# Kernel tuning notes

Measured on AMD Instinct MI355X. Metric: run time of the kernel, lower is better.

Reference implementation:

```python
import jax, jax.numpy as jnp
import numpy as np

EMBED_DIM = 1024
NUM_HEADS = 16
HEAD_DIM = EMBED_DIM // NUM_HEADS
EPS = 1e-5


def setup_inputs() -> dict:
    key = jax.random.key(0)
    ks = jax.random.split(key, 14)
    B, S, E = 2, 2048, EMBED_DIM
    s = 1.0 / np.sqrt(E)
    inp = {
        "x": jax.random.normal(ks[0], (B, S, E), dtype=jnp.float32),
        "Wq": jax.random.normal(ks[1], (E, E), dtype=jnp.float32) * s,
        "bq": jax.random.normal(ks[2], (E,), dtype=jnp.float32) * 0.01,
        "Wk": jax.random.normal(ks[3], (E, E), dtype=jnp.float32) * s,
        "bk": jax.random.normal(ks[4], (E,), dtype=jnp.float32) * 0.01,
        "Wv": jax.random.normal(ks[5], (E, E), dtype=jnp.float32) * s,
        "bv": jax.random.normal(ks[6], (E,), dtype=jnp.float32) * 0.01,
        "Wo": jax.random.normal(ks[7], (E, E), dtype=jnp.float32) * s,
        "bo": jax.random.normal(ks[8], (E,), dtype=jnp.float32) * 0.01,
        "qn_w": jnp.ones((HEAD_DIM,), jnp.float32) + 0.1 * jax.random.normal(ks[9], (HEAD_DIM,), jnp.float32),
        "qn_b": 0.1 * jax.random.normal(ks[10], (HEAD_DIM,), jnp.float32),
        "kn_w": jnp.ones((HEAD_DIM,), jnp.float32) + 0.1 * jax.random.normal(ks[11], (HEAD_DIM,), jnp.float32),
        "kn_b": 0.1 * jax.random.normal(ks[12], (HEAD_DIM,), jnp.float32),
    }
    return inp


def _layernorm(t, w, b):
    # normalize over last axis (head_dim), matching eqx.nn.LayerNorm(eps=1e-5)
    mu = jnp.mean(t, axis=-1, keepdims=True)
    var = jnp.mean(jnp.square(t - mu), axis=-1, keepdims=True)
    return (t - mu) * jax.lax.rsqrt(var + EPS) * w + b


def reference(x, Wq, bq, Wk, bk, Wv, bv, Wo, bo, qn_w, qn_b, kn_w, kn_b):
    B, S, E = x.shape
    H, D = NUM_HEADS, HEAD_DIM
    q = (x @ Wq.T + bq).reshape(B, S, H, D)
    k = (x @ Wk.T + bk).reshape(B, S, H, D)
    v = (x @ Wv.T + bv).reshape(B, S, H, D)
    q = _layernorm(q, qn_w, qn_b)
    k = _layernorm(k, kn_w, kn_b)
    scale = D ** (-0.5)
    # [B,H,S,S] score matrix (faithful to naive implementation)
    scores = jnp.einsum("bqhd,bkhd->bhqk", q, k) * scale
    attn = jax.nn.softmax(scores, axis=-1)
    out = jnp.einsum("bhqk,bkhd->bqhd", attn, v).reshape(B, S, E)
    return out @ Wo.T + bo
```

## Files before the change

kernel.cpp:

```cpp
#include <hip/hip_runtime.h>
#include <stdint.h>


typedef __bf16 bf16_t;
typedef __bf16 bf16x8 __attribute__((ext_vector_type(8)));
typedef __bf16 bf16x4 __attribute__((ext_vector_type(4)));
typedef __bf16 bf16x2 __attribute__((ext_vector_type(2)));
typedef float f32x4 __attribute__((ext_vector_type(4)));
typedef float f32x16 __attribute__((ext_vector_type(16)));
typedef uint32_t u32x4 __attribute__((ext_vector_type(4)));

#define S_LEN 2048

__device__ __forceinline__ void load_lds16(const void* g, void* l) {
  __builtin_amdgcn_global_load_lds((__attribute__((address_space(1))) void*)g,
                                   (__attribute__((address_space(3))) void*)l,
                                   16, 0, 0);
}

__device__ __forceinline__ f32x4 mfma16(bf16x8 a, bf16x8 b, f32x4 c) {
  return __builtin_amdgcn_mfma_f32_16x16x32_bf16(a, b, c, 0, 0, 0);
}

__device__ __forceinline__ f32x16 mfma32(bf16x8 a, bf16x8 b, f32x16 c) {
  return __builtin_amdgcn_mfma_f32_32x32x16_bf16(a, b, c, 0, 0, 0);
}

__device__ __forceinline__ uint32_t pk_bf16(float a, float b) {
  bf16x2 v; v[0] = (bf16_t)a; v[1] = (bf16_t)b;
  return __builtin_bit_cast(uint32_t, v);
}

__device__ __forceinline__ void plswap(uint32_t& a, uint32_t& b) {
  asm volatile("v_permlane32_swap_b32 %0, %1" : "+v"(a), "+v"(b));
}

__global__ void cvt_bf16(const float* __restrict__ in, bf16_t* __restrict__ out, int n) {
  int i = (blockIdx.x * blockDim.x + threadIdx.x) * 4;
  if (i >= n) return;
  float4 v = *reinterpret_cast<const float4*>(in + i);
  bf16x4 o;
  o[0] = (bf16_t)v.x; o[1] = (bf16_t)v.y; o[2] = (bf16_t)v.z; o[3] = (bf16_t)v.w;
  *reinterpret_cast<bf16x4*>(out + i) = o;
}

__device__ __forceinline__ void gemm_main(const bf16_t* __restrict__ ga,
                                          const bf16_t* __restrict__ gb,
                                          bf16_t* As, bf16_t* Bs,
                                          int t, int wr, int wc, int lg, int lr,
                                          f32x4 (&acc)[4][4]) {
  for (int k0 = 0; k0 < 1024; k0 += 32) {
    load_lds16(ga + k0,          As + t * 8);
    load_lds16(ga + 65536 + k0,  As + 2048 + t * 8);
    load_lds16(gb + k0,          Bs + t * 8);
    load_lds16(gb + 65536 + k0,  Bs + 2048 + t * 8);
    __syncthreads();
    bf16x8 af[4], bfr[4];
#pragma unroll
    for (int mt = 0; mt < 4; ++mt)
      af[mt] = *reinterpret_cast<const bf16x8*>(As + ((wr * 64 + mt * 16 + lr) << 5) + lg * 8);
#pragma unroll
    for (int nt = 0; nt < 4; ++nt)
      bfr[nt] = *reinterpret_cast<const bf16x8*>(Bs + ((wc * 64 + nt * 16 + lr) << 5) + lg * 8);
#pragma unroll
    for (int mt = 0; mt < 4; ++mt)
#pragma unroll
      for (int nt = 0; nt < 4; ++nt)
        acc[mt][nt] = mfma16(af[mt], bfr[nt], acc[mt][nt]);
    __syncthreads();
  }
}

__launch_bounds__(256, 2)
__global__ void gemm_qkv_ln(const bf16_t* __restrict__ A, const bf16_t* __restrict__ Bt,
                            const float* __restrict__ bq, const float* __restrict__ bk,
                            const float* __restrict__ bv,
                            const float* __restrict__ qnw, const float* __restrict__ qnb,
                            const float* __restrict__ knw, const float* __restrict__ knb,
                            bf16_t* __restrict__ Qb, bf16_t* __restrict__ Kb,
                            bf16_t* __restrict__ Vt) {
  __shared__ alignas(16) bf16_t As[128 * 32];
  __shared__ alignas(16) bf16_t Bs[128 * 32];
  const int t = threadIdx.x;
  const int bm = blockIdx.y, bn = blockIdx.x;
  const int w = t >> 6, lane = t & 63;
  const int wr = w >> 1, wc = w & 1;
  const int lg = lane >> 4, lr = lane & 15;

  f32x4 acc[4][4] = {};
  const int srow = t >> 2;
  const int scol = (t & 3) << 3;
  const bf16_t* ga = A + ((size_t)(bm * 128 + srow) << 10) + scol;
  const bf16_t* gb = Bt + ((size_t)(bn * 128 + srow) << 10) + scol;
  gemm_main(ga, gb, As, Bs, t, wr, wc, lg, lr, acc);

  const int nbase = bn * 128 + wc * 64;
  const int region = nbase >> 10;
  const int h = (nbase & 1023) >> 6;

  if (region == 2) {
#pragma unroll
    for (int mt = 0; mt < 4; ++mt)
#pragma unroll
      for (int r = 0; r < 4; ++r) {
        const int gm = bm * 128 + wr * 64 + mt * 16 + lg * 4 + r;
        const int b = gm >> 11, s = gm & 2047;
#pragma unroll
        for (int nt = 0; nt < 4; ++nt) {
          const int d = nt * 16 + lr;
          float val = acc[mt][nt][r] + bv[h * 64 + d];
          Vt[((size_t)((b * 16 + h) * 64 + d) << 11) + s] = (bf16_t)val;
        }
      }
  } else {
    const float* bias = region ? bk : bq;
    const float* lw = region ? knw : qnw;
    const float* lb = region ? knb : qnb;
    bf16_t* Outp = region ? Kb : Qb;
#pragma unroll
    for (int mt = 0; mt < 4; ++mt)
#pragma unroll
      for (int r = 0; r < 4; ++r) {
        const int gm = bm * 128 + wr * 64 + mt * 16 + lg * 4 + r;
        const int b = gm >> 11, s = gm & 2047;
        float vv[4], sum = 0.f, sumsq = 0.f;
#pragma unroll
        for (int nt = 0; nt < 4; ++nt) {
          const int d = nt * 16 + lr;
          vv[nt] = acc[mt][nt][r] + bias[h * 64 + d];
          sum += vv[nt];
          sumsq += vv[nt] * vv[nt];
        }
#pragma unroll
        for (int mk = 1; mk < 16; mk <<= 1) {
          sum += __shfl_xor(sum, mk);
          sumsq += __shfl_xor(sumsq, mk);
        }
        const float mean = sum * (1.f / 64.f);
        const float var = sumsq * (1.f / 64.f) - mean * mean;
        const float rstd = rsqrtf(var + 1e-5f);
        const size_t rowoff = ((size_t)((b * 16 + h) * 2048 + s)) << 6;
#pragma unroll
        for (int nt = 0; nt < 4; ++nt) {
          const int d = nt * 16 + lr;
          float y = (vv[nt] - mean) * rstd * lw[d] + lb[d];
          Outp[rowoff + d] = (bf16_t)y;
        }
      }
  }
}

__launch_bounds__(256, 2)
__global__ void gemm_out(const bf16_t* __restrict__ A, const bf16_t* __restrict__ Bt,
                         const float* __restrict__ bo, float* __restrict__ dout) {
  __shared__ alignas(16) bf16_t As[128 * 32];
  __shared__ alignas(16) bf16_t Bs[128 * 32];
  const int t = threadIdx.x;
  const int bm = blockIdx.y, bn = blockIdx.x;
  const int w = t >> 6, lane = t & 63;
  const int wr = w >> 1, wc = w & 1;
  const int lg = lane >> 4, lr = lane & 15;

  f32x4 acc[4][4] = {};
  const int srow = t >> 2;
  const int scol = (t & 3) << 3;
  const bf16_t* ga = A + ((size_t)(bm * 128 + srow) << 10) + scol;
  const bf16_t* gb = Bt + ((size_t)(bn * 128 + srow) << 10) + scol;
  gemm_main(ga, gb, As, Bs, t, wr, wc, lg, lr, acc);

#pragma unroll
  for (int mt = 0; mt < 4; ++mt)
#pragma unroll
    for (int r = 0; r < 4; ++r) {
      const int gm = bm * 128 + wr * 64 + mt * 16 + lg * 4 + r;
#pragma unroll
      for (int nt = 0; nt < 4; ++nt) {
        const int gn = bn * 128 + wc * 64 + nt * 16 + lr;
        dout[((size_t)gm << 10) + gn] = acc[mt][nt][r] + bo[gn];
      }
    }
}

__launch_bounds__(256, 2)
__global__ void attn_kernel(const bf16_t* __restrict__ Qb, const bf16_t* __restrict__ Kb,
                            const bf16_t* __restrict__ Vt, bf16_t* __restrict__ Og) {
  __shared__ alignas(16) bf16_t Ks[2][64 * 64];
  __shared__ alignas(16) bf16_t Vs[2][64 * 64];

  const int t = threadIdx.x;
  const int w = t >> 6, lane = t & 63;
  const int lq = lane & 31;
  const int hi = lane >> 5;
  const int bh = blockIdx.y;
  const int b = bh >> 4, h = bh & 15;
  const int q0 = blockIdx.x * 128 + w * 32;

  bf16x8 qf[4];
  {
    const bf16_t* qp = Qb + (((size_t)bh * S_LEN + q0 + lq) << 6) + hi * 8;
#pragma unroll
    for (int c = 0; c < 4; ++c)
      qf[c] = *reinterpret_cast<const bf16x8*>(qp + c * 16);
  }

  f32x16 oacc0 = {}, oacc1 = {};
  float m_ = -1e30f, l_ = 0.f;
  const float sc = 0.125f * 1.44269504f;

  const int sr = t >> 3;
  const int ssw = ((t & 7) ^ (sr & 7)) << 3;
  const bf16_t* kbase = Kb + (((size_t)bh * S_LEN) << 6);
  const bf16_t* vbase = Vt + ((size_t)bh << 17);

#define STAGE(buf, j)                                                        \
  {                                                                          \
    const bf16_t* kb = kbase + ((size_t)((j) * 64) << 6);                    \
    const bf16_t* vb = vbase + (j) * 64;                                     \
    load_lds16(kb + (sr << 6) + ssw,        &Ks[buf][t * 8]);                \
    load_lds16(kb + ((sr + 32) << 6) + ssw, &Ks[buf][2048 + t * 8]);         \
    load_lds16(vb + sr * S_LEN + ssw,        &Vs[buf][t * 8]);               \
    load_lds16(vb + (sr + 32) * S_LEN + ssw, &Vs[buf][2048 + t * 8]);        \
  }

  STAGE(0, 0);
  __syncthreads();

  for (int j = 0; j < 32; ++j) {
    const int cur = j & 1;
    if (j < 31) STAGE(cur ^ 1, j + 1);

    f32x16 sa0, sa1;
    {
      f32x16 z0 = {}, z1 = {};
      const int row0 = lq, row1 = 32 + lq;
      const bf16_t* kr0 = &Ks[cur][row0 << 6];
      const bf16_t* kr1 = &Ks[cur][row1 << 6];
      const int sw0 = row0 & 7, sw1 = row1 & 7;
#pragma unroll
      for (int c = 0; c < 4; ++c) {
        bf16x8 kf0 = *reinterpret_cast<const bf16x8*>(kr0 + (((c * 2 + hi) ^ sw0) << 3));
        z0 = mfma32(kf0, qf[c], z0);
      }
#pragma unroll
      for (int c = 0; c < 4; ++c) {
        bf16x8 kf1 = *reinterpret_cast<const bf16x8*>(kr1 + (((c * 2 + hi) ^ sw1) << 3));
        z1 = mfma32(kf1, qf[c], z1);
      }
      sa0 = z0; sa1 = z1;
    }

    float mv[16];
#pragma unroll
    for (int i = 0; i < 16; ++i) mv[i] = fmaxf(sa0[i], sa1[i]);
#pragma unroll
    for (int s2 = 8; s2 >= 1; s2 >>= 1)
#pragma unroll
      for (int i = 0; i < s2; ++i) mv[i] = fmaxf(mv[i], mv[i + s2]);
    float mx = fmaxf(mv[0], __shfl_xor(mv[0], 32));
    const float ms = mx * sc;

    if (__any(ms > m_ + 8.f)) {
      const float mn = fmaxf(m_, ms);
      const float alpha = __builtin_amdgcn_exp2f(m_ - mn);
      oacc0 *= alpha; oacc1 *= alpha;
      l_ *= alpha;
      m_ = mn;
    }

    const float mneg = -m_;
    f32x16 p0, p1;
#pragma unroll
    for (int i = 0; i < 16; ++i) p0[i] = __builtin_amdgcn_exp2f(__builtin_fmaf(sa0[i], sc, mneg));
#pragma unroll
    for (int i = 0; i < 16; ++i) p1[i] = __builtin_amdgcn_exp2f(__builtin_fmaf(sa1[i], sc, mneg));

    float sv[16];
#pragma unroll
    for (int i = 0; i < 16; ++i) sv[i] = p0[i] + p1[i];
#pragma unroll
    for (int s2 = 8; s2 >= 1; s2 >>= 1)
#pragma unroll
      for (int i = 0; i < s2; ++i) sv[i] += sv[i + s2];
    l_ += sv[0] + __shfl_xor(sv[0], 32);

#pragma unroll
    for (int c = 0; c < 4; ++c) {
      const f32x16 ph = (c < 2) ? p0 : p1;
      const int cl = c & 1;
      uint32_t w00 = pk_bf16(ph[8 * cl + 0], ph[8 * cl + 1]);
      uint32_t w01 = pk_bf16(ph[8 * cl + 2], ph[8 * cl + 3]);
      uint32_t w10 = pk_bf16(ph[8 * cl + 4], ph[8 * cl + 5]);
      uint32_t w11 = pk_bf16(ph[8 * cl + 6], ph[8 * cl + 7]);
      plswap(w00, w10);
      plswap(w01, w11);
      u32x4 pw = {w00, w01, w10, w11};
      bf16x8 pf = __builtin_bit_cast(bf16x8, pw);
      {
        const int vrow = lq;
        bf16x8 vf = *reinterpret_cast<const bf16x8*>(
            &Vs[cur][(vrow << 6) + (((c * 2 + hi) ^ (vrow & 7)) << 3)]);
        oacc0 = mfma32(vf, pf, oacc0);
      }
      {
        const int vrow = 32 + lq;
        bf16x8 vf = *reinterpret_cast<const bf16x8*>(
            &Vs[cur][(vrow << 6) + (((c * 2 + hi) ^ (vrow & 7)) << 3)]);
        oacc1 = mfma32(vf, pf, oacc1);
      }
    }
    __syncthreads();
  }

  __syncthreads();
  bf16_t* Os = &Ks[0][0] + w * 2048;
  const float inv = __builtin_amdgcn_rcpf(l_);
#pragma unroll
  for (int dh = 0; dh < 2; ++dh) {
    const f32x16 oa = dh ? oacc1 : oacc0;
#pragma unroll
    for (int g = 0; g < 8; ++g) {
      const int reg = g * 2;
      const int dl = (reg & 3) + 8 * (reg >> 2) + 4 * hi;
      const int d = dh * 32 + dl;
      const uint32_t wv = pk_bf16(oa[reg] * inv, oa[reg + 1] * inv);
      const int byte = lq * 128 + ((((d >> 3) ^ (lq & 7))) << 4) + ((d & 7) << 1);
      *reinterpret_cast<uint32_t*>(reinterpret_cast<char*>(Os) + byte) = wv;
    }
  }
#pragma unroll
  for (int it = 0; it < 4; ++it) {
    const int q = it * 8 + (lane >> 3);
    const int ch = lane & 7;
    bf16x8 ov = *reinterpret_cast<const bf16x8*>(
        reinterpret_cast<char*>(Os) + q * 128 + ((ch ^ (q & 7)) << 4));
    const size_t gaddr = (((size_t)(b * S_LEN + q0 + q)) << 10) + h * 64 + ch * 8;
    *reinterpret_cast<bf16x8*>(Og + gaddr) = ov;
  }
#undef STAGE
}

extern "C" void kernel_launch(void* const* d_in, const int* in_sizes, int n_in,
                              void* d_out, int out_size, void* d_ws, size_t ws_size,
                              hipStream_t stream) {
  const float* x = (const float*)d_in[0];
  const float* Wq = (const float*)d_in[1];
  const float* bq = (const float*)d_in[2];
  const float* Wk = (const float*)d_in[3];
  const float* bk = (const float*)d_in[4];
  const float* Wv = (const float*)d_in[5];
  const float* bv = (const float*)d_in[6];
  const float* Wo = (const float*)d_in[7];
  const float* bo = (const float*)d_in[8];
  const float* qnw = (const float*)d_in[9];
  const float* qnb = (const float*)d_in[10];
  const float* knw = (const float*)d_in[11];
  const float* knb = (const float*)d_in[12];
  float* out = (float*)d_out;

  uint8_t* ws = (uint8_t*)d_ws;
  bf16_t* xb = (bf16_t*)(ws + 0);
  bf16_t* Wb = (bf16_t*)(ws + 8388608);
  bf16_t* Wob = (bf16_t*)(ws + 14680064);
  bf16_t* Qb = (bf16_t*)(ws + 16777216);
  bf16_t* Kb = (bf16_t*)(ws + 25165824);
  bf16_t* Vt = (bf16_t*)(ws + 33554432);
  bf16_t* Ob = (bf16_t*)(ws + 41943040);

  cvt_bf16<<<4096, 256, 0, stream>>>(x, xb, 4194304);
  cvt_bf16<<<1024, 256, 0, stream>>>(Wq, Wb, 1048576);
  cvt_bf16<<<1024, 256, 0, stream>>>(Wk, Wb + 1048576, 1048576);
  cvt_bf16<<<1024, 256, 0, stream>>>(Wv, Wb + 2097152, 1048576);
  cvt_bf16<<<1024, 256, 0, stream>>>(Wo, Wob, 1048576);

  gemm_qkv_ln<<<dim3(24, 32), 256, 0, stream>>>(xb, Wb, bq, bk, bv, qnw, qnb, knw, knb,
                                                Qb, Kb, Vt);
  attn_kernel<<<dim3(16, 32), 256, 0, stream>>>(Qb, Kb, Vt, Ob);
  gemm_out<<<dim3(8, 32), 256, 0, stream>>>(Ob, Wob, bo, out);
}
```

Measured before the change: 138.5 us.

## Split attention over KV halves, merge convert launches, shrink output GEMM tiles

Attention now splits the key/value sequence into two halves across a grid z-dimension, with more blocks per CU, and writes fp32 partial outputs plus max and sum statistics. A new combine kernel merges the two halves into bf16. The five conversion launches become one kernel, and the output GEMM uses 64-row M tiles to double its block count. These changes target the under-filled GPU, where 512 attention blocks and 256 GEMM blocks leave CUs idle, at the cost of extra fp32 traffic and one more launch. The split path runs only if the workspace is large enough.

```diff
diff --git a/kernel.cpp b/kernel.cpp
--- a/kernel.cpp
+++ b/kernel.cpp
@@ -35,13 +35,27 @@
   asm volatile("v_permlane32_swap_b32 %0, %1" : "+v"(a), "+v"(b));
 }
 
-__global__ void cvt_bf16(const float* __restrict__ in, bf16_t* __restrict__ out, int n) {
-  int i = (blockIdx.x * blockDim.x + threadIdx.x) * 4;
-  if (i >= n) return;
-  float4 v = *reinterpret_cast<const float4*>(in + i);
+__global__ void cvt_all(const float* __restrict__ x, const float* __restrict__ Wq,
+                        const float* __restrict__ Wk, const float* __restrict__ Wv,
+                        const float* __restrict__ Wo,
+                        bf16_t* __restrict__ xb, bf16_t* __restrict__ Wb,
+                        bf16_t* __restrict__ Wob) {
+  const int bid = blockIdx.x;
+  const float* src; bf16_t* dst; int idx;
+  if (bid < 4096) { src = x; dst = xb; idx = bid; }
+  else {
+    const int r = bid - 4096, rg = r >> 10;
+    idx = r & 1023;
+    if (rg == 0)      { src = Wq; dst = Wb; }
+    else if (rg == 1) { src = Wk; dst = Wb + (1 << 20); }
+    else if (rg == 2) { src = Wv; dst = Wb + (2 << 20); }
+    else              { src = Wo; dst = Wob; }
+  }
+  const int i = (idx * 256 + threadIdx.x) * 4;
+  float4 v = *reinterpret_cast<const float4*>(src + i);
   bf16x4 o;
   o[0] = (bf16_t)v.x; o[1] = (bf16_t)v.y; o[2] = (bf16_t)v.z; o[3] = (bf16_t)v.w;
-  *reinterpret_cast<bf16x4*>(out + i) = o;
+  *reinterpret_cast<bf16x4*>(dst + i) = o;
 }
 
 __device__ __forceinline__ void gemm_main(const bf16_t* __restrict__ ga,
@@ -153,7 +167,7 @@
 __launch_bounds__(256, 2)
 __global__ void gemm_out(const bf16_t* __restrict__ A, const bf16_t* __restrict__ Bt,
                          const float* __restrict__ bo, float* __restrict__ dout) {
-  __shared__ alignas(16) bf16_t As[128 * 32];
+  __shared__ alignas(16) bf16_t As[64 * 32];
   __shared__ alignas(16) bf16_t Bs[128 * 32];
   const int t = threadIdx.x;
   const int bm = blockIdx.y, bn = blockIdx.x;
@@ -161,18 +175,37 @@
   const int wr = w >> 1, wc = w & 1;
   const int lg = lane >> 4, lr = lane & 15;
 
-  f32x4 acc[4][4] = {};
+  f32x4 acc[2][4] = {};
   const int srow = t >> 2;
   const int scol = (t & 3) << 3;
-  const bf16_t* ga = A + ((size_t)(bm * 128 + srow) << 10) + scol;
+  const bf16_t* ga = A + ((size_t)(bm * 64 + srow) << 10) + scol;
   const bf16_t* gb = Bt + ((size_t)(bn * 128 + srow) << 10) + scol;
-  gemm_main(ga, gb, As, Bs, t, wr, wc, lg, lr, acc);
-
-#pragma unroll
-  for (int mt = 0; mt < 4; ++mt)
+
+  for (int k0 = 0; k0 < 1024; k0 += 32) {
+    load_lds16(ga + k0,          As + t * 8);
+    load_lds16(gb + k0,          Bs + t * 8);
+    load_lds16(gb + 65536 + k0,  Bs + 2048 + t * 8);
+    __syncthreads();
+    bf16x8 af[2], bfr[4];
+#pragma unroll
+    for (int mt = 0; mt < 2; ++mt)
+      af[mt] = *reinterpret_cast<const bf16x8*>(As + ((wr * 32 + mt * 16 + lr) << 5) + lg * 8);
+#pragma unroll
+    for (int nt = 0; nt < 4; ++nt)
+      bfr[nt] = *reinterpret_cast<const bf16x8*>(Bs + ((wc * 64 + nt * 16 + lr) << 5) + lg * 8);
+#pragma unroll
+    for (int mt = 0; mt < 2; ++mt)
+#pragma unroll
+      for (int nt = 0; nt < 4; ++nt)
+        acc[mt][nt] = mfma16(af[mt], bfr[nt], acc[mt][nt]);
+    __syncthreads();
+  }
+
+#pragma unroll
+  for (int mt = 0; mt < 2; ++mt)
 #pragma unroll
     for (int r = 0; r < 4; ++r) {
-      const int gm = bm * 128 + wr * 64 + mt * 16 + lg * 4 + r;
+      const int gm = bm * 64 + wr * 32 + mt * 16 + lg * 4 + r;
 #pragma unroll
       for (int nt = 0; nt < 4; ++nt) {
         const int gn = bn * 128 + wc * 64 + nt * 16 + lr;
@@ -181,19 +214,22 @@
     }
 }
 
-__launch_bounds__(256, 2)
+template <int NSPLIT>
+__launch_bounds__(256, 4)
 __global__ void attn_kernel(const bf16_t* __restrict__ Qb, const bf16_t* __restrict__ Kb,
-                            const bf16_t* __restrict__ Vt, bf16_t* __restrict__ Og) {
-  __shared__ alignas(16) bf16_t Ks[2][64 * 64];
-  __shared__ alignas(16) bf16_t Vs[2][64 * 64];
+                            const bf16_t* __restrict__ Vt, bf16_t* __restrict__ Og,
+                            float* __restrict__ Op, float* __restrict__ Ml) {
+  __shared__ alignas(16) bf16_t KVs[4][64 * 64];
 
   const int t = threadIdx.x;
   const int w = t >> 6, lane = t & 63;
   const int lq = lane & 31;
   const int hi = lane >> 5;
   const int bh = blockIdx.y;
+  const int z = (NSPLIT == 1) ? 0 : blockIdx.z;
   const int b = bh >> 4, h = bh & 15;
   const int q0 = blockIdx.x * 128 + w * 32;
+  const int ntiles = 32 / NSPLIT;
 
   bf16x8 qf[4];
   {
@@ -212,29 +248,29 @@
   const bf16_t* kbase = Kb + (((size_t)bh * S_LEN) << 6);
   const bf16_t* vbase = Vt + ((size_t)bh << 17);
 
-#define STAGE(buf, j)                                                        \
+#define STAGE(buf, jt)                                                       \
   {                                                                          \
-    const bf16_t* kb = kbase + ((size_t)((j) * 64) << 6);                    \
-    const bf16_t* vb = vbase + (j) * 64;                                     \
-    load_lds16(kb + (sr << 6) + ssw,        &Ks[buf][t * 8]);                \
-    load_lds16(kb + ((sr + 32) << 6) + ssw, &Ks[buf][2048 + t * 8]);         \
-    load_lds16(vb + sr * S_LEN + ssw,        &Vs[buf][t * 8]);               \
-    load_lds16(vb + (sr + 32) * S_LEN + ssw, &Vs[buf][2048 + t * 8]);        \
-  }
-
-  STAGE(0, 0);
+    const bf16_t* kb = kbase + ((size_t)((jt) * 64) << 6);                   \
+    const bf16_t* vb = vbase + (jt) * 64;                                    \
+    load_lds16(kb + (sr << 6) + ssw,        &KVs[buf][t * 8]);               \
+    load_lds16(kb + ((sr + 32) << 6) + ssw, &KVs[buf][2048 + t * 8]);        \
+    load_lds16(vb + sr * S_LEN + ssw,        &KVs[2 + (buf)][t * 8]);        \
+    load_lds16(vb + (sr + 32) * S_LEN + ssw, &KVs[2 + (buf)][2048 + t * 8]); \
+  }
+
+  STAGE(0, z * ntiles);
   __syncthreads();
 
-  for (int j = 0; j < 32; ++j) {
+  for (int j = 0; j < ntiles; ++j) {
     const int cur = j & 1;
-    if (j < 31) STAGE(cur ^ 1, j + 1);
+    if (j < ntiles - 1) STAGE(cur ^ 1, z * ntiles + j + 1);
 
     f32x16 sa0, sa1;
     {
       f32x16 z0 = {}, z1 = {};
       const int row0 = lq, row1 = 32 + lq;
-      const bf16_t* kr0 = &Ks[cur][row0 << 6];
-      const bf16_t* kr1 = &Ks[cur][row1 << 6];
+      const bf16_t* kr0 = &KVs[cur][row0 << 6];
+      const bf16_t* kr1 = &KVs[cur][row1 << 6];
       const int sw0 = row0 & 7, sw1 = row1 & 7;
 #pragma unroll
       for (int c = 0; c < 4; ++c) {
@@ -298,45 +334,95 @@
       {
         const int vrow = lq;
         bf16x8 vf = *reinterpret_cast<const bf16x8*>(
-            &Vs[cur][(vrow << 6) + (((c * 2 + hi) ^ (vrow & 7)) << 3)]);
+            &KVs[2 + cur][(vrow << 6) + (((c * 2 + hi) ^ (vrow & 7)) << 3)]);
         oacc0 = mfma32(vf, pf, oacc0);
       }
       {
         const int vrow = 32 + lq;
         bf16x8 vf = *reinterpret_cast<const bf16x8*>(
-            &Vs[cur][(vrow << 6) + (((c * 2 + hi) ^ (vrow & 7)) << 3)]);
+            &KVs[2 + cur][(vrow << 6) + (((c * 2 + hi) ^ (vrow & 7)) << 3)]);
         oacc1 = mfma32(vf, pf, oacc1);
       }
     }
     __syncthreads();
   }
 
-  __syncthreads();
-  bf16_t* Os = &Ks[0][0] + w * 2048;
-  const float inv = __builtin_amdgcn_rcpf(l_);
-#pragma unroll
-  for (int dh = 0; dh < 2; ++dh) {
-    const f32x16 oa = dh ? oacc1 : oacc0;
-#pragma unroll
-    for (int g = 0; g < 8; ++g) {
-      const int reg = g * 2;
-      const int dl = (reg & 3) + 8 * (reg >> 2) + 4 * hi;
-      const int d = dh * 32 + dl;
-      const uint32_t wv = pk_bf16(oa[reg] * inv, oa[reg + 1] * inv);
-      const int byte = lq * 128 + ((((d >> 3) ^ (lq & 7))) << 4) + ((d & 7) << 1);
-      *reinterpret_cast<uint32_t*>(reinterpret_cast<char*>(Os) + byte) = wv;
-    }
-  }
-#pragma unroll
-  for (int it = 0; it < 4; ++it) {
-    const int q = it * 8 + (lane >> 3);
-    const int ch = lane & 7;
-    bf16x8 ov = *reinterpret_cast<const bf16x8*>(
-        reinterpret_cast<char*>(Os) + q * 128 + ((ch ^ (q & 7)) << 4));
-    const size_t gaddr = (((size_t)(b * S_LEN + q0 + q)) << 10) + h * 64 + ch * 8;
-    *reinterpret_cast<bf16x8*>(Og + gaddr) = ov;
+  if constexpr (NSPLIT == 1) {
+    bf16_t* Os = &KVs[0][0] + w * 2048;
+    const float inv = __builtin_amdgcn_rcpf(l_);
+#pragma unroll
+    for (int dh = 0; dh < 2; ++dh) {
+      const f32x16 oa = dh ? oacc1 : oacc0;
+#pragma unroll
+      for (int g = 0; g < 8; ++g) {
+        const int reg = g * 2;
+        const int dl = (reg & 3) + 8 * (reg >> 2) + 4 * hi;
+        const int d = dh * 32 + dl;
+        const uint32_t wv = pk_bf16(oa[reg] * inv, oa[reg + 1] * inv);
+        const int byte = lq * 128 + ((((d >> 3) ^ (lq & 7))) << 4) + ((d & 7) << 1);
+        *reinterpret_cast<uint32_t*>(reinterpret_cast<char*>(Os) + byte) = wv;
+      }
+    }
+#pragma unroll
+    for (int it = 0; it < 4; ++it) {
+      const int q = it * 8 + (lane >> 3);
+      const int ch = lane & 7;
+      bf16x8 ov = *reinterpret_cast<const bf16x8*>(
+          reinterpret_cast<char*>(Os) + q * 128 + ((ch ^ (q & 7)) << 4));
+      const size_t gaddr = (((size_t)(b * S_LEN + q0 + q)) << 10) + h * 64 + ch * 8;
+      *reinterpret_cast<bf16x8*>(Og + gaddr) = ov;
+    }
+  } else {
+    float* Os32 = reinterpret_cast<float*>(&KVs[0][0]) + w * 2048;
+#pragma unroll
+    for (int dh = 0; dh < 2; ++dh) {
+      const f32x16 oa = dh ? oacc1 : oacc0;
+#pragma unroll
+      for (int reg = 0; reg < 16; ++reg) {
+        const int dl = (reg & 3) + 8 * (reg >> 2) + 4 * hi;
+        const int d = dh * 32 + dl;
+        Os32[lq * 64 + (((d >> 2) ^ (lq & 15)) << 2) + (d & 3)] = oa[reg];
+      }
+    }
+    if (lane < 32) {
+      float2 mlv; mlv.x = m_; mlv.y = l_;
+      *reinterpret_cast<float2*>(Ml + (((size_t)(z * 32 + bh) * 2048 + q0 + lq) << 1)) = mlv;
+    }
+#pragma unroll
+    for (int it = 0; it < 4; ++it) {
+      const int q = it * 8 + (lane >> 3);
+      const size_t rowoff = ((size_t)((z * 32 + bh) * 2048 + q0 + q)) << 6;
+#pragma unroll
+      for (int c2 = 0; c2 < 2; ++c2) {
+        const int ch = ((lane & 7) << 1) + c2;
+        f32x4 v = *reinterpret_cast<const f32x4*>(Os32 + q * 64 + ((ch ^ (q & 15)) << 2));
+        *reinterpret_cast<f32x4*>(Op + rowoff + (ch << 2)) = v;
+      }
+    }
   }
 #undef STAGE
+}
+
+__global__ void attn_combine(const float* __restrict__ Op, const float* __restrict__ Ml,
+                             bf16_t* __restrict__ Ob) {
+  const int gid = blockIdx.x * 256 + threadIdx.x;
+  const int row = gid >> 4, ch = gid & 15;
+  const float* o1 = Op + ((size_t)row << 6) + ch * 4;
+  const float* o2 = o1 + (1u << 22);
+  const float2 a1 = *reinterpret_cast<const float2*>(Ml + row * 2);
+  const float2 a2 = *reinterpret_cast<const float2*>(Ml + (1u << 17) + row * 2);
+  const float mmax = fmaxf(a1.x, a2.x);
+  const float w1 = __builtin_amdgcn_exp2f(a1.x - mmax);
+  const float w2 = __builtin_amdgcn_exp2f(a2.x - mmax);
+  const float inv = 1.f / (a1.y * w1 + a2.y * w2);
+  f32x4 v1 = *reinterpret_cast<const f32x4*>(o1);
+  f32x4 v2 = *reinterpret_cast<const f32x4*>(o2);
+  bf16x4 o;
+#pragma unroll
+  for (int i = 0; i < 4; ++i) o[i] = (bf16_t)((v1[i] * w1 + v2[i] * w2) * inv);
+  const int bh = row >> 11, s = row & 2047;
+  const int b = bh >> 4, h = bh & 15;
+  *reinterpret_cast<bf16x4*>(Ob + (((size_t)(b * S_LEN + s)) << 10) + h * 64 + ch * 4) = o;
 }
 
 extern "C" void kernel_launch(void* const* d_in, const int* in_sizes, int n_in,
@@ -365,15 +451,19 @@
   bf16_t* Kb = (bf16_t*)(ws + 25165824);
   bf16_t* Vt = (bf16_t*)(ws + 33554432);
   bf16_t* Ob = (bf16_t*)(ws + 41943040);
-
-  cvt_bf16<<<4096, 256, 0, stream>>>(x, xb, 4194304);
-  cvt_bf16<<<1024, 256, 0, stream>>>(Wq, Wb, 1048576);
-  cvt_bf16<<<1024, 256, 0, stream>>>(Wk, Wb + 1048576, 1048576);
-  cvt_bf16<<<1024, 256, 0, stream>>>(Wv, Wb + 2097152, 1048576);
-  cvt_bf16<<<1024, 256, 0, stream>>>(Wo, Wob, 1048576);
+  float*  Opart = (float*)(ws + 50331648);
+  float*  Mlp   = (float*)(ws + 83886080);
+  const bool split = ws_size >= 84934656ull;
+
+  cvt_all<<<8192, 256, 0, stream>>>(x, Wq, Wk, Wv, Wo, xb, Wb, Wob);
 
   gemm_qkv_ln<<<dim3(24, 32), 256, 0, stream>>>(xb, Wb, bq, bk, bv, qnw, qnb, knw, knb,
                                                 Qb, Kb, Vt);
-  attn_kernel<<<dim3(16, 32), 256, 0, stream>>>(Qb, Kb, Vt, Ob);
-  gemm_out<<<dim3(8, 32), 256, 0, stream>>>(Ob, Wob, bo, out);
-}
+  if (split) {
+    attn_kernel<2><<<dim3(16, 32, 2), 256, 0, stream>>>(Qb, Kb, Vt, Ob, Opart, Mlp);
+    attn_combine<<<4096, 256, 0, stream>>>(Opart, Mlp, Ob);
+  } else {
+    attn_kernel<1><<<dim3(16, 32, 1), 256, 0, stream>>>(Qb, Kb, Vt, Ob, Opart, Mlp);
+  }
+  gemm_out<<<dim3(8, 64), 256, 0, stream>>>(Ob, Wob, bo, out);
+}
```

Measured after the change: 131.6 us. -4.9%, faster.
